# Kernel tuning notes

Hardware: AMD Instinct MI355X
Metric: run time of the kernel (lower is better)

Reference implementation:

```python
import jax, jax.numpy as jnp
import numpy as np

DT = 0.01  # time-grid spacing


def _get_A(ts, omega_sq, gamma_0, gamma_amp, omega_d):
    # ts: [...]; returns [..., 2, 2] system matrix A(t)
    gamma = gamma_0 * (1.0 + gamma_amp * jnp.sin(omega_d * ts))
    z = jnp.zeros_like(ts)
    o = jnp.ones_like(ts)
    row0 = jnp.stack([z, o], axis=-1)
    row1 = jnp.stack([-omega_sq * o, -gamma], axis=-1)
    return jnp.stack([row0, row1], axis=-2)


def _expm2x2(M):
    # Closed-form matrix exponential for batched 2x2 matrices [..., 2, 2].
    a, b = M[..., 0, 0], M[..., 0, 1]
    c, d = M[..., 1, 0], M[..., 1, 1]
    m = 0.5 * (a + d)                 # trace/2
    det = a * d - b * c
    delta = m * m - det               # discriminant
    s = jnp.sqrt(jnp.abs(delta))
    pos = delta >= 0
    small = s < 1e-6
    s_safe = jnp.where(small, 1.0, s)
    cosl = jnp.where(pos, jnp.cosh(s), jnp.cos(s))
    sinch = jnp.where(small, 1.0,
                      jnp.where(pos, jnp.sinh(s_safe), jnp.sin(s_safe)) / s_safe)
    I = jnp.eye(2, dtype=M.dtype)
    em = jnp.exp(m)[..., None, None]
    return em * (cosl[..., None, None] * I
                 + sinch[..., None, None] * (M - m[..., None, None] * I))


def setup_inputs() -> dict:
    key = jax.random.key(0)
    k1, = jax.random.split(key, 1)
    T, B = 8192, 4096
    t = jnp.arange(T, dtype=jnp.float32) * DT
    x0 = jax.random.normal(k1, (2, B), dtype=jnp.float32)
    return {
        "t": t,
        "x0": x0,
        "omega_sq": jnp.float32(1.2),
        "gamma_0": jnp.float32(0.35),
        "gamma_amp": jnp.float32(0.15),
        "omega_d": jnp.float32(1.1),
        "use_commutator": 1,
    }


def reference(t, x0, omega_sq, gamma_0, gamma_amp, omega_d, use_commutator):
    t0 = t[:-1]                      # [T-1]
    dt = t[1:] - t[:-1]              # [T-1]
    A0 = _get_A(t0, omega_sq, gamma_0, gamma_amp, omega_d)
    A_mid = _get_A(t0 + dt / 2, omega_sq, gamma_0, gamma_amp, omega_d)
    A1 = _get_A(t0 + dt, omega_sq, gamma_0, gamma_amp, omega_d)
    Omega = A_mid * dt[:, None, None]               # Magnus-1 term
    if use_commutator:
        comm = A0 @ A1 - A1 @ A0                    # [T-1, 2, 2]
        Omega = Omega + (dt ** 2 / 12.0)[:, None, None] * comm
    E = _expm2x2(Omega)                             # [T-1, 2, 2] propagators

    def step(x, Ei):
        xn = Ei @ x                                 # [2, B]
        return xn, xn

    _, ys = jax.lax.scan(step, x0, E)
    return jnp.concatenate([x0[None], ys], axis=0)  # [T, 2, B]
```

## Files before the change

kernel.cpp:

```cpp
#include <hip/hip_runtime.h>


struct M2 { float a, b, c, d; };

__device__ __forceinline__ M2 mmul(const M2& X, const M2& Y) {
    M2 r;
    r.a = X.a * Y.a + X.b * Y.c;
    r.b = X.a * Y.b + X.b * Y.d;
    r.c = X.c * Y.a + X.d * Y.c;
    r.d = X.c * Y.b + X.d * Y.d;
    return r;
}

__device__ __forceinline__ M2 build_E(const float* __restrict__ t, int n,
                                      float w2, float g0, float ga, float wd,
                                      int uc) {
    float t0 = t[n], t1 = t[n + 1];
    float dt = t1 - t0;
    float tm = t0 + dt * 0.5f;

    float gam0 = g0 * (1.0f + ga * sinf(wd * t0));
    float gamm = g0 * (1.0f + ga * sinf(wd * tm));
    float gam1 = g0 * (1.0f + ga * sinf(wd * t1));

    float Oa = 0.0f;
    float Ob = dt;
    float Oc = -w2 * dt;
    float Od = -gamm * dt;
    if (uc) {
        float k = dt * dt * (1.0f / 12.0f);
        float del = gam0 - gam1;
        Ob += k * del;
        Oc += k * (w2 * del);
    }

    float m   = 0.5f * (Oa + Od);
    float det = Oa * Od - Ob * Oc;
    float delta = m * m - det;
    float s = sqrtf(fabsf(delta));
    bool pos = delta >= 0.0f;
    bool small_ = s < 1e-6f;
    float s_safe = small_ ? 1.0f : s;
    float cosl = pos ? coshf(s) : cosf(s);
    float sn   = pos ? sinhf(s_safe) : sinf(s_safe);
    float sinch = small_ ? 1.0f : sn / s_safe;
    float em = expf(m);

    M2 E;
    E.a = em * (cosl + sinch * (Oa - m));
    E.b = em * (sinch * Ob);
    E.c = em * (sinch * Oc);
    E.d = em * (cosl + sinch * (Od - m));
    return E;
}

__global__ __launch_bounds__(1024) void escan_kernel(const float* __restrict__ t,
                                                     const float* __restrict__ p_w2,
                                                     const float* __restrict__ p_g0,
                                                     const float* __restrict__ p_ga,
                                                     const float* __restrict__ p_wd,
                                                     const int* __restrict__ p_uc,
                                                     float4* __restrict__ P, int T) {
    __shared__ float4 lds[1024];
    const int j = threadIdx.x;
    const int base = j * 8;

    float w2 = *p_w2, g0 = *p_g0, ga = *p_ga, wd = *p_wd;
    int uc = *p_uc;

    M2 S[8];
    #pragma unroll
    for (int mi = 0; mi < 8; ++mi) {
        int k = base + mi;
        M2 Mk;
        if (k < T - 1) {
            Mk = build_E(t, k, w2, g0, ga, wd, uc);
        } else {
            Mk.a = 1.0f; Mk.b = 0.0f; Mk.c = 0.0f; Mk.d = 1.0f;
        }
        S[mi] = (mi == 0) ? Mk : mmul(Mk, S[mi - 1]);
    }

    M2 acc = S[7];
    lds[j] = make_float4(acc.a, acc.b, acc.c, acc.d);
    for (int d = 1; d < 1024; d <<= 1) {
        __syncthreads();
        M2 prev;
        bool act = (j >= d);
        if (act) {
            float4 p = lds[j - d];
            prev.a = p.x; prev.b = p.y; prev.c = p.z; prev.d = p.w;
        }
        __syncthreads();
        if (act) {
            acc = mmul(acc, prev);
            lds[j] = make_float4(acc.a, acc.b, acc.c, acc.d);
        }
    }
    __syncthreads();

    M2 Bm;
    if (j == 0) { Bm.a = 1.0f; Bm.b = 0.0f; Bm.c = 0.0f; Bm.d = 1.0f; }
    else {
        float4 p = lds[j - 1];
        Bm.a = p.x; Bm.b = p.y; Bm.c = p.z; Bm.d = p.w;
    }

    if (j == 0) P[0] = make_float4(1.0f, 0.0f, 0.0f, 1.0f);
    #pragma unroll
    for (int mi = 0; mi < 8; ++mi) {
        int g = base + mi + 1;
        if (g < T) {
            M2 r = mmul(S[mi], Bm);
            P[g] = make_float4(r.a, r.b, r.c, r.d);
        }
    }
}

__global__ __launch_bounds__(256) void out_kernel(const float4* __restrict__ P,
                                                  const float* __restrict__ x0,
                                                  float* __restrict__ out,
                                                  int B, int T) {
    const int q = B >> 2;
    const float4* xr0 = (const float4*)x0;
    const float4* xr1 = xr0 + q;
    const int n0 = blockIdx.x * 2;
    const int n1 = n0 + 1;
    const bool has1 = (n1 < T);

    const float4 p0 = P[n0];
    const float4 p1 = has1 ? P[n1] : p0;

    float4* o0 = (float4*)(out + (size_t)n0 * (size_t)(2 * B));
    float4* o1 = (float4*)(out + (size_t)n1 * (size_t)(2 * B));

    for (int g = threadIdx.x; g < q; g += 256) {
        float4 u = xr0[g];
        float4 v = xr1[g];
        float4 r;

        r.x = p0.x * u.x + p0.y * v.x;
        r.y = p0.x * u.y + p0.y * v.y;
        r.z = p0.x * u.z + p0.y * v.z;
        r.w = p0.x * u.w + p0.y * v.w;
        o0[g] = r;
        r.x = p0.z * u.x + p0.w * v.x;
        r.y = p0.z * u.y + p0.w * v.y;
        r.z = p0.z * u.z + p0.w * v.z;
        r.w = p0.z * u.w + p0.w * v.w;
        o0[q + g] = r;

        if (has1) {
            r.x = p1.x * u.x + p1.y * v.x;
            r.y = p1.x * u.y + p1.y * v.y;
            r.z = p1.x * u.z + p1.y * v.z;
            r.w = p1.x * u.w + p1.y * v.w;
            o1[g] = r;
            r.x = p1.z * u.x + p1.w * v.x;
            r.y = p1.z * u.y + p1.w * v.y;
            r.z = p1.z * u.z + p1.w * v.z;
            r.w = p1.z * u.w + p1.w * v.w;
            o1[q + g] = r;
        }
    }
}

extern "C" void kernel_launch(void* const* d_in, const int* in_sizes, int n_in,
                              void* d_out, int out_size, void* d_ws, size_t ws_size,
                              hipStream_t stream) {
    const float* t   = (const float*)d_in[0];
    const float* x0  = (const float*)d_in[1];
    const float* w2  = (const float*)d_in[2];
    const float* g0  = (const float*)d_in[3];
    const float* ga  = (const float*)d_in[4];
    const float* wd  = (const float*)d_in[5];
    const int*   uc  = (const int*)d_in[6];

    const int T = in_sizes[0];
    const int B = in_sizes[1] / 2;

    float4* P = (float4*)d_ws;
    float* out = (float*)d_out;

    escan_kernel<<<1, 1024, 0, stream>>>(t, w2, g0, ga, wd, uc, P, T);
    out_kernel<<<(T + 1) / 2, 256, 0, stream>>>(P, x0, out, B, T);
}
```

Measured before the change: 284.2 us.

## Replace single-block scan with per-block chunk-product reduction in output kernel

Drops the single-workgroup 1024-thread Hillis-Steele scan, which runs on one CU and is fully serialised before the output kernel. The first kernel now only computes 8-step chunk products across many blocks. Each output block rebuilds its own prefix propagator by tree-reducing up to 1024 chunk matrices in LDS and applying a few leftover step matrices. This trades a serial latency-bound stage for redundant reduction work, extra syncs and a serial tail in every one of the ~4096 output blocks, and it changes the floating-point association order.

```diff
diff --git a/kernel.cpp b/kernel.cpp
--- a/kernel.cpp
+++ b/kernel.cpp
@@ -11,6 +11,10 @@
     r.d = X.c * Y.b + X.d * Y.d;
     return r;
 }
+
+__device__ __forceinline__ M2 ident() { M2 r; r.a = 1.f; r.b = 0.f; r.c = 0.f; r.d = 1.f; return r; }
+__device__ __forceinline__ float4 m2f4(const M2& m) { return make_float4(m.a, m.b, m.c, m.d); }
+__device__ __forceinline__ M2 f4m2(const float4& v) { M2 m; m.a = v.x; m.b = v.y; m.c = v.z; m.d = v.w; return m; }
 
 __device__ __forceinline__ M2 build_E(const float* __restrict__ t, int n,
                                       float w2, float g0, float ga, float wd,
@@ -54,87 +58,98 @@
     return E;
 }
 
-__global__ __launch_bounds__(1024) void escan_kernel(const float* __restrict__ t,
-                                                     const float* __restrict__ p_w2,
-                                                     const float* __restrict__ p_g0,
-                                                     const float* __restrict__ p_ga,
-                                                     const float* __restrict__ p_wd,
-                                                     const int* __restrict__ p_uc,
-                                                     float4* __restrict__ P, int T) {
-    __shared__ float4 lds[1024];
-    const int j = threadIdx.x;
-    const int base = j * 8;
-
+__global__ void chunk_kernel(const float* __restrict__ t,
+                             const float* __restrict__ p_w2,
+                             const float* __restrict__ p_g0,
+                             const float* __restrict__ p_ga,
+                             const float* __restrict__ p_wd,
+                             const int* __restrict__ p_uc,
+                             float4* __restrict__ C, int T, int NC) {
+    int j = blockIdx.x * blockDim.x + threadIdx.x;
+    if (j >= NC) return;
     float w2 = *p_w2, g0 = *p_g0, ga = *p_ga, wd = *p_wd;
     int uc = *p_uc;
 
-    M2 S[8];
+    int base = j * 8;
+    M2 S = ident();
     #pragma unroll
     for (int mi = 0; mi < 8; ++mi) {
         int k = base + mi;
-        M2 Mk;
-        if (k < T - 1) {
-            Mk = build_E(t, k, w2, g0, ga, wd, uc);
-        } else {
-            Mk.a = 1.0f; Mk.b = 0.0f; Mk.c = 0.0f; Mk.d = 1.0f;
-        }
-        S[mi] = (mi == 0) ? Mk : mmul(Mk, S[mi - 1]);
-    }
-
-    M2 acc = S[7];
-    lds[j] = make_float4(acc.a, acc.b, acc.c, acc.d);
-    for (int d = 1; d < 1024; d <<= 1) {
-        __syncthreads();
-        M2 prev;
-        bool act = (j >= d);
-        if (act) {
-            float4 p = lds[j - d];
-            prev.a = p.x; prev.b = p.y; prev.c = p.z; prev.d = p.w;
-        }
-        __syncthreads();
-        if (act) {
-            acc = mmul(acc, prev);
-            lds[j] = make_float4(acc.a, acc.b, acc.c, acc.d);
-        }
-    }
-    __syncthreads();
-
-    M2 Bm;
-    if (j == 0) { Bm.a = 1.0f; Bm.b = 0.0f; Bm.c = 0.0f; Bm.d = 1.0f; }
-    else {
-        float4 p = lds[j - 1];
-        Bm.a = p.x; Bm.b = p.y; Bm.c = p.z; Bm.d = p.w;
-    }
-
-    if (j == 0) P[0] = make_float4(1.0f, 0.0f, 0.0f, 1.0f);
-    #pragma unroll
-    for (int mi = 0; mi < 8; ++mi) {
-        int g = base + mi + 1;
-        if (g < T) {
-            M2 r = mmul(S[mi], Bm);
-            P[g] = make_float4(r.a, r.b, r.c, r.d);
-        }
-    }
-}
-
-__global__ __launch_bounds__(256) void out_kernel(const float4* __restrict__ P,
+        if (k < T - 1) S = mmul(build_E(t, k, w2, g0, ga, wd, uc), S);
+    }
+    C[j] = m2f4(S);
+}
+
+__global__ __launch_bounds__(256) void out_kernel(const float* __restrict__ t,
+                                                  const float* __restrict__ p_w2,
+                                                  const float* __restrict__ p_g0,
+                                                  const float* __restrict__ p_ga,
+                                                  const float* __restrict__ p_wd,
+                                                  const int* __restrict__ p_uc,
+                                                  const float4* __restrict__ C,
                                                   const float* __restrict__ x0,
                                                   float* __restrict__ out,
                                                   int B, int T) {
+    __shared__ float4 red[256];
+    __shared__ float4 aux[2];
+
+    const int tid = threadIdx.x;
+    const int n0 = blockIdx.x * 2;
+    const int n1 = n0 + 1;
+    const bool has1 = (n1 < T);
+    const int cj = n0 >> 3;
+    const int r0 = n0 & 7;
+
+    if (tid == 255) {
+        float w2 = *p_w2, g0 = *p_g0, ga = *p_ga, wd = *p_wd;
+        int uc = *p_uc;
+        int base = cj * 8;
+        M2 W = ident();
+        for (int i = 0; i < r0; ++i) W = mmul(build_E(t, base + i, w2, g0, ga, wd, uc), W);
+        M2 El = ident();
+        if (has1) El = build_E(t, base + r0, w2, g0, ga, wd, uc);
+        aux[0] = m2f4(W);
+        aux[1] = m2f4(El);
+    }
+
+    {
+        int k0 = tid * 4;
+        M2 L = ident();
+        #pragma unroll
+        for (int l = 0; l < 4; ++l) {
+            int k = k0 + l;
+            if (k < cj) L = mmul(f4m2(C[k]), L);
+        }
+        red[tid] = m2f4(L);
+    }
+    __syncthreads();
+
+    for (int s = 128; s > 0; s >>= 1) {
+        if (tid < s) red[tid] = m2f4(mmul(f4m2(red[tid + s]), f4m2(red[tid])));
+        __syncthreads();
+    }
+
+    if (tid == 0) {
+        M2 Q  = f4m2(red[0]);
+        M2 W  = f4m2(aux[0]);
+        M2 El = f4m2(aux[1]);
+        M2 P0 = mmul(W, Q);
+        M2 P1 = mmul(El, P0);
+        red[0] = m2f4(P0);
+        red[1] = m2f4(P1);
+    }
+    __syncthreads();
+
+    const float4 p0 = red[0];
+    const float4 p1 = red[1];
+
     const int q = B >> 2;
     const float4* xr0 = (const float4*)x0;
     const float4* xr1 = xr0 + q;
-    const int n0 = blockIdx.x * 2;
-    const int n1 = n0 + 1;
-    const bool has1 = (n1 < T);
-
-    const float4 p0 = P[n0];
-    const float4 p1 = has1 ? P[n1] : p0;
-
     float4* o0 = (float4*)(out + (size_t)n0 * (size_t)(2 * B));
     float4* o1 = (float4*)(out + (size_t)n1 * (size_t)(2 * B));
 
-    for (int g = threadIdx.x; g < q; g += 256) {
+    for (int g = tid; g < q; g += 256) {
         float4 u = xr0[g];
         float4 v = xr1[g];
         float4 r;
@@ -179,9 +194,10 @@
     const int T = in_sizes[0];
     const int B = in_sizes[1] / 2;
 
-    float4* P = (float4*)d_ws;
+    const int NC = (T - 1 + 7) / 8;
+    float4* C = (float4*)d_ws;
     float* out = (float*)d_out;
 
-    escan_kernel<<<1, 1024, 0, stream>>>(t, w2, g0, ga, wd, uc, P, T);
-    out_kernel<<<(T + 1) / 2, 256, 0, stream>>>(P, x0, out, B, T);
-}
+    chunk_kernel<<<(NC + 255) / 256, 256, 0, stream>>>(t, w2, g0, ga, wd, uc, C, T, NC);
+    out_kernel<<<(T + 1) / 2, 256, 0, stream>>>(t, w2, g0, ga, wd, uc, C, x0, out, B, T);
+}
```

After: 278.6 us. 1.02x faster.
